# Optimization experiments

Measured on AMD Instinct MI355X. Metric: run time of the kernel, lower is better.

## Reference

```python
import math
import jax, jax.numpy as jnp
import numpy as np

B, Q, K = 1, 2048, 2048
CQ = CK = CV = 128
H, CH = 8, 32
HD = H * CH  # 256


def setup_inputs() -> dict:
    key = jax.random.key(0)
    ks = jax.random.split(key, 12)
    s = 0.02
    return {
        "q_x": jax.random.normal(ks[0], (B, Q, CQ), jnp.float32),
        "kv_x": jax.random.normal(ks[1], (B, K, CK), jnp.float32),
        "bias": jax.random.normal(ks[2], (B, 1, Q, K), jnp.float32),
        "distance": jax.random.uniform(ks[3], (B, Q, K, H), jnp.float32),
        "Wq": jax.random.normal(ks[4], (CQ, HD), jnp.float32) * s,
        "Wk": jax.random.normal(ks[5], (CK, HD), jnp.float32) * s,
        "Wv": jax.random.normal(ks[6], (CV, HD), jnp.float32) * s,
        "Wg": jax.random.normal(ks[7], (CQ, HD), jnp.float32) * s,
        "bg": jnp.zeros((HD,), jnp.float32),
        "Wo": jax.random.normal(ks[8], (HD, CQ), jnp.float32) * s,
        "bo": jnp.zeros((CQ,), jnp.float32),
    }


def reference(q_x, kv_x, bias, distance, Wq, Wk, Wv, Wg, bg, Wo, bo):
    # Projections -> [B, S, H, CH]
    q = (q_x @ Wq).reshape(B, Q, H, CH) / math.sqrt(CH)
    k = (kv_x @ Wk).reshape(B, K, H, CH)
    v = (kv_x @ Wv).reshape(B, K, H, CH)
    # Scores [B, H, Q, K]
    a = jnp.einsum("bqhc,bkhc->bhqk", q, k)
    a = a + bias
    # mha_permu=True: distance [B,Q,K,H] -> [B,H,Q,K]; rel_dis_pair_bias='add'
    a = a + jnp.transpose(distance, (0, 3, 1, 2))
    a = jax.nn.softmax(a, axis=-1)
    o = jnp.einsum("bhqk,bkhc->bqhc", a, v)  # [B, Q, H, CH]
    # Gating
    g = jax.nn.sigmoid(q_x @ Wg + bg).reshape(B, Q, H, CH)
    o = o * g
    o = o.reshape(B, Q, HD)
    return o @ Wo + bo
```

## Files before the change

### kernel.cpp

```cpp
#include <hip/hip_runtime.h>
#include <hip/hip_bf16.h>

#define Qn 2048
#define Kn 2048
#define Cin 128
#define Hn 8
#define CHn 32
#define HDn 256
#define NSPLIT 8

typedef __attribute__((ext_vector_type(8))) short short8;
typedef __attribute__((ext_vector_type(4))) float f32x4;

static __device__ __forceinline__ unsigned short f2bf(float f) {
    unsigned int u = __float_as_uint(f);
    u += 0x7fffu + ((u >> 16) & 1u);
    return (unsigned short)(u >> 16);
}

static __device__ __forceinline__ void ld16(const void* g, void* l) {
    __builtin_amdgcn_global_load_lds(
        (const __attribute__((address_space(1))) void*)g,
        (__attribute__((address_space(3))) void*)l, 16, 0, 0);
}

__global__ __launch_bounds__(256) void proj_kernel(
    const float* __restrict__ qx, const float* __restrict__ kvx,
    const float* __restrict__ Wq, const float* __restrict__ Wk,
    const float* __restrict__ Wv, const float* __restrict__ Wg,
    const float* __restrict__ bg,
    unsigned short* __restrict__ qb, unsigned short* __restrict__ kb,
    unsigned short* __restrict__ vtb, float* __restrict__ gb)
{
    const int mat = blockIdx.y;
    const int r0 = blockIdx.x * 8;
    const int j = threadIdx.x;
    const float* A = (mat == 0 || mat == 3) ? qx : kvx;
    const float* W = (mat == 0) ? Wq : (mat == 1) ? Wk : (mat == 2) ? Wv : Wg;
    const float* Ar = A + r0 * Cin;
    float acc[8] = {0.f, 0.f, 0.f, 0.f, 0.f, 0.f, 0.f, 0.f};
    for (int c = 0; c < Cin; ++c) {
        const float w = W[c * HDn + j];
        #pragma unroll
        for (int i = 0; i < 8; ++i)
            acc[i] = fmaf(Ar[i * Cin + c], w, acc[i]);
    }
    if (mat == 0) {
        const float s = 0.17677669529663687f;
        #pragma unroll
        for (int i = 0; i < 8; ++i)
            qb[(r0 + i) * HDn + j] = f2bf(acc[i] * s);
    } else if (mat == 1) {
        #pragma unroll
        for (int i = 0; i < 8; ++i)
            kb[(r0 + i) * HDn + j] = f2bf(acc[i]);
    } else if (mat == 2) {
        unsigned short tmp[8];
        #pragma unroll
        for (int i = 0; i < 8; ++i) tmp[i] = f2bf(acc[i]);
        *(short8*)(vtb + (size_t)j * Kn + r0) = *(short8*)tmp;
    } else {
        const float b = bg[j];
        #pragma unroll
        for (int i = 0; i < 8; ++i)
            gb[(r0 + i) * HDn + j] = 1.f / (1.f + __expf(-(acc[i] + b)));
    }
}

__global__ __launch_bounds__(512, 4) void attn_kernel(
    const unsigned short* __restrict__ qb, const unsigned short* __restrict__ kb,
    const unsigned short* __restrict__ vtb,
    const float* __restrict__ bias, const float* __restrict__ dist,
    float* __restrict__ opart, float* __restrict__ lpart)
{
    __shared__ float dlds[2][16][32][8];
    __shared__ float blds[2][16][32];
    __shared__ unsigned short ps[Hn][16][40];

    const int bx = blockIdx.x;
    const int qt = bx >> 3;
    const int sp = bx & 7;
    const int q0 = qt * 16;
    const int k00 = sp * 256;
    const int t = threadIdx.x;
    const int h = t >> 6;
    const int l = t & 63;
    const int g = l >> 4;
    const int n = l & 15;

    const short8 qf = *(const short8*)(qb + (q0 + n) * HDn + h * CHn + g * 8);

    f32x4 o0 = {0.f, 0.f, 0.f, 0.f};
    f32x4 o1 = {0.f, 0.f, 0.f, 0.f};
    float lacc[4] = {0.f, 0.f, 0.f, 0.f};
    unsigned short* psh = &ps[h][0][0];
    const f32x4 z = {0.f, 0.f, 0.f, 0.f};

    const float* dsrcA = dist + (size_t)(q0 + h) * Kn * Hn + l * 4;
    const float* dsrcB = dist + (size_t)(q0 + h + 8) * Kn * Hn + l * 4;
    const float* bsrc  = bias + (size_t)(q0 + h * 8 + (l >> 3)) * Kn + (l & 7) * 4;

    short8 kf[2][2], vf[2][2];

    #define STAGE(buf, kt_) do {                                              \
        const int k0s = k00 + (kt_) * 32;                                     \
        ld16(dsrcA + (size_t)k0s * 8, &dlds[buf][h][0][0]);                   \
        ld16(dsrcB + (size_t)k0s * 8, &dlds[buf][h + 8][0][0]);               \
        if (h < 2) ld16(bsrc + k0s, &blds[buf][h * 8][0]);                    \
    } while (0)

    #define KVLOAD(set, kt_) do {                                             \
        const int k0v = k00 + (kt_) * 32;                                     \
        kf[set][0] = *(const short8*)(kb + (k0v + n) * HDn + h * CHn + g * 8);      \
        kf[set][1] = *(const short8*)(kb + (k0v + 16 + n) * HDn + h * CHn + g * 8); \
        vf[set][0] = *(const short8*)(vtb + (h * CHn + n) * Kn + k0v + g * 8);      \
        vf[set][1] = *(const short8*)(vtb + (h * CHn + 16 + n) * Kn + k0v + g * 8); \
    } while (0)

    KVLOAD(0, 0);
    __builtin_amdgcn_sched_barrier(0);
    STAGE(0, 0);

    #pragma unroll
    for (int kt = 0; kt < 8; ++kt) {
        const int cur = kt & 1;
        asm volatile("s_waitcnt vmcnt(0)\n\ts_barrier" ::: "memory");
        if (kt < 7) {
            KVLOAD(cur ^ 1, kt + 1);
            __builtin_amdgcn_sched_barrier(0);
            STAGE(cur ^ 1, kt + 1);
            __builtin_amdgcn_sched_barrier(0);
        }
        f32x4 sf[2];
        sf[0] = __builtin_amdgcn_mfma_f32_16x16x32_bf16(qf, kf[cur][0], z, 0, 0, 0);
        sf[1] = __builtin_amdgcn_mfma_f32_16x16x32_bf16(qf, kf[cur][1], z, 0, 0, 0);
        #pragma unroll
        for (int kk = 0; kk < 2; ++kk) {
            #pragma unroll
            for (int r = 0; r < 4; ++r) {
                const float p = __expf(sf[kk][r]
                                       + dlds[cur][g * 4 + r][kk * 16 + n][h]
                                       + blds[cur][g * 4 + r][kk * 16 + n]);
                sf[kk][r] = p;
                lacc[r] += p;
                psh[(g * 4 + r) * 40 + kk * 16 + n] = f2bf(p);
            }
        }
        const short8 pf = *(const short8*)(psh + n * 40 + g * 8);
        o0 = __builtin_amdgcn_mfma_f32_16x16x32_bf16(pf, vf[cur][0], o0, 0, 0, 0);
        o1 = __builtin_amdgcn_mfma_f32_16x16x32_bf16(pf, vf[cur][1], o1, 0, 0, 0);
    }
    #undef STAGE
    #undef KVLOAD

    float* op = opart + (size_t)sp * (Qn * HDn);
    #pragma unroll
    for (int r = 0; r < 4; ++r) {
        const int qg = q0 + g * 4 + r;
        op[qg * HDn + h * CHn + n] = o0[r];
        op[qg * HDn + h * CHn + 16 + n] = o1[r];
        float v = lacc[r];
        v += __shfl_xor(v, 1);
        v += __shfl_xor(v, 2);
        v += __shfl_xor(v, 4);
        v += __shfl_xor(v, 8);
        lacc[r] = v;
    }
    if (n == 0) {
        float* lp = lpart + (size_t)sp * (Qn * Hn);
        #pragma unroll
        for (int r = 0; r < 4; ++r)
            lp[(q0 + g * 4 + r) * Hn + h] = lacc[r];
    }
}

__global__ __launch_bounds__(256) void mergeout_kernel(
    const float* __restrict__ opart, const float* __restrict__ lpart,
    const float* __restrict__ gb, const float* __restrict__ Wo,
    const float* __restrict__ bo, float* __restrict__ out)
{
    __shared__ float olds[HDn];
    __shared__ float red[4][128];
    const int q = blockIdx.x;
    const int t = threadIdx.x;
    const int h = t >> 5;
    float s = 0.f;
    #pragma unroll
    for (int sp = 0; sp < NSPLIT; ++sp)
        s += opart[(size_t)sp * (Qn * HDn) + q * HDn + t];
    float lt = 0.f;
    #pragma unroll
    for (int sp = 0; sp < NSPLIT; ++sp)
        lt += lpart[(size_t)sp * (Qn * Hn) + q * Hn + h];
    olds[t] = (s / lt) * gb[q * HDn + t];
    __syncthreads();
    const int p = t & 63;
    const int seg = t >> 6;
    float a0 = 0.f, a1 = 0.f;
    for (int c = seg * 64; c < seg * 64 + 64; ++c) {
        const float ov = olds[c];
        const float2 w = *(const float2*)(Wo + c * Cin + 2 * p);
        a0 = fmaf(ov, w.x, a0);
        a1 = fmaf(ov, w.y, a1);
    }
    red[seg][2 * p] = a0;
    red[seg][2 * p + 1] = a1;
    __syncthreads();
    if (t < 128)
        out[q * Cin + t] = red[0][t] + red[1][t] + red[2][t] + red[3][t] + bo[t];
}

extern "C" void kernel_launch(void* const* d_in, const int* in_sizes, int n_in,
                              void* d_out, int out_size, void* d_ws, size_t ws_size,
                              hipStream_t stream)
{
    const float* qx   = (const float*)d_in[0];
    const float* kvx  = (const float*)d_in[1];
    const float* bias = (const float*)d_in[2];
    const float* dist = (const float*)d_in[3];
    const float* Wq   = (const float*)d_in[4];
    const float* Wk   = (const float*)d_in[5];
    const float* Wv   = (const float*)d_in[6];
    const float* Wg   = (const float*)d_in[7];
    const float* bg   = (const float*)d_in[8];
    const float* Wo   = (const float*)d_in[9];
    const float* bo   = (const float*)d_in[10];
    float* out = (float*)d_out;

    char* w = (char*)d_ws;
    unsigned short* qb  = (unsigned short*)(w);
    unsigned short* kb  = (unsigned short*)(w + (1ull << 20));
    unsigned short* vtb = (unsigned short*)(w + (2ull << 20));
    float* gb    = (float*)(w + (3ull << 20));
    float* opart = (float*)(w + (5ull << 20));
    float* lpart = (float*)(w + (21ull << 20));

    proj_kernel<<<dim3(Qn / 8, 4), 256, 0, stream>>>(qx, kvx, Wq, Wk, Wv, Wg, bg, qb, kb, vtb, gb);
    attn_kernel<<<dim3(128 * NSPLIT), 512, 0, stream>>>(qb, kb, vtb, bias, dist, opart, lpart);
    mergeout_kernel<<<dim3(Qn), 256, 0, stream>>>(opart, lpart, gb, Wo, bo, out);
}
```

Measured before the change: 279.1 us.

## Triple-buffer distance tiles with transposed padded LDS layout and preload bias

Distance tiles are now staged with 4-byte global-to-LDS loads that transpose them into a head-major, padded layout (stride 260). This is meant to remove LDS bank conflicts when each head reads its distance values. The staging is triple-buffered with a two-tile lookahead, and partial vmcnt waits replace full drains so loads overlap compute. The whole 256-key bias slice is loaded once up front. The cost is four times as many load instructions with smaller transfers, plus more LDS use, which could lower occupancy.

Measured after the change: 313.7 us. 1.12x slower.

```diff
diff --git a/kernel.cpp b/kernel.cpp
--- a/kernel.cpp
+++ b/kernel.cpp
@@ -8,6 +8,8 @@
 #define CHn 32
 #define HDn 256
 #define NSPLIT 8
+#define DSTR 260
+#define DBUF (16 * DSTR)
 
 typedef __attribute__((ext_vector_type(8))) short short8;
 typedef __attribute__((ext_vector_type(4))) float f32x4;
@@ -22,6 +24,11 @@
     __builtin_amdgcn_global_load_lds(
         (const __attribute__((address_space(1))) void*)g,
         (__attribute__((address_space(3))) void*)l, 16, 0, 0);
+}
+static __device__ __forceinline__ void ld4(const void* g, void* l) {
+    __builtin_amdgcn_global_load_lds(
+        (const __attribute__((address_space(1))) void*)g,
+        (__attribute__((address_space(3))) void*)l, 4, 0, 0);
 }
 
 __global__ __launch_bounds__(256) void proj_kernel(
@@ -73,8 +80,8 @@
     const float* __restrict__ bias, const float* __restrict__ dist,
     float* __restrict__ opart, float* __restrict__ lpart)
 {
-    __shared__ float dlds[2][16][32][8];
-    __shared__ float blds[2][16][32];
+    __shared__ float dl[3 * DBUF];
+    __shared__ float bl[16 * DSTR];
     __shared__ unsigned short ps[Hn][16][40];
 
     const int bx = blockIdx.x;
@@ -96,56 +103,69 @@
     unsigned short* psh = &ps[h][0][0];
     const f32x4 z = {0.f, 0.f, 0.f, 0.f};
 
-    const float* dsrcA = dist + (size_t)(q0 + h) * Kn * Hn + l * 4;
-    const float* dsrcB = dist + (size_t)(q0 + h + 8) * Kn * Hn + l * 4;
-    const float* bsrc  = bias + (size_t)(q0 + h * 8 + (l >> 3)) * Kn + (l & 7) * 4;
+    const int dloff = (l & 31) * 8 + (l >> 5);
+    const float* dgA = dist + (size_t)(q0 + h) * Kn * Hn;
+    const float* dgB = dist + (size_t)(q0 + h + 8) * Kn * Hn;
 
     short8 kf[2][2], vf[2][2];
 
     #define STAGE(buf, kt_) do {                                              \
-        const int k0s = k00 + (kt_) * 32;                                     \
-        ld16(dsrcA + (size_t)k0s * 8, &dlds[buf][h][0][0]);                   \
-        ld16(dsrcB + (size_t)k0s * 8, &dlds[buf][h + 8][0][0]);               \
-        if (h < 2) ld16(bsrc + k0s, &blds[buf][h * 8][0]);                    \
+        const float* gA_ = dgA + (size_t)(k00 + (kt_) * 32) * Hn + dloff;     \
+        const float* gB_ = dgB + (size_t)(k00 + (kt_) * 32) * Hn + dloff;     \
+        float* lA_ = dl + (buf) * DBUF + h * DSTR;                            \
+        float* lB_ = dl + (buf) * DBUF + (h + 8) * DSTR;                      \
+        _Pragma("unroll") for (int i_ = 0; i_ < 4; ++i_) {                    \
+            ld4(gA_ + 2 * i_, lA_ + i_ * 64);                                 \
+            ld4(gB_ + 2 * i_, lB_ + i_ * 64);                                 \
+        }                                                                     \
     } while (0)
 
     #define KVLOAD(set, kt_) do {                                             \
-        const int k0v = k00 + (kt_) * 32;                                     \
+        const int k0v = k00 + (kt_) * 32;                                      \
         kf[set][0] = *(const short8*)(kb + (k0v + n) * HDn + h * CHn + g * 8);      \
         kf[set][1] = *(const short8*)(kb + (k0v + 16 + n) * HDn + h * CHn + g * 8); \
         vf[set][0] = *(const short8*)(vtb + (h * CHn + n) * Kn + k0v + g * 8);      \
         vf[set][1] = *(const short8*)(vtb + (h * CHn + 16 + n) * Kn + k0v + g * 8); \
     } while (0)
 
+    ld16(bias + (size_t)(q0 + 2 * h) * Kn + k00 + l * 4, bl + (2 * h) * DSTR);
+    ld16(bias + (size_t)(q0 + 2 * h + 1) * Kn + k00 + l * 4, bl + (2 * h + 1) * DSTR);
+    __builtin_amdgcn_sched_barrier(0);
+    STAGE(0, 0);
+    __builtin_amdgcn_sched_barrier(0);
     KVLOAD(0, 0);
     __builtin_amdgcn_sched_barrier(0);
-    STAGE(0, 0);
+    STAGE(1, 1);
+    __builtin_amdgcn_sched_barrier(0);
 
     #pragma unroll
     for (int kt = 0; kt < 8; ++kt) {
+        const int cb = kt % 3;
         const int cur = kt & 1;
-        asm volatile("s_waitcnt vmcnt(0)\n\ts_barrier" ::: "memory");
-        if (kt < 7) {
-            KVLOAD(cur ^ 1, kt + 1);
-            __builtin_amdgcn_sched_barrier(0);
-            STAGE(cur ^ 1, kt + 1);
-            __builtin_amdgcn_sched_barrier(0);
-        }
+        if (kt < 7) asm volatile("s_waitcnt vmcnt(8)\n\ts_barrier" ::: "memory");
+        else        asm volatile("s_waitcnt vmcnt(4)\n\ts_barrier" ::: "memory");
+        if (kt < 7) { KVLOAD(cur ^ 1, kt + 1); __builtin_amdgcn_sched_barrier(0); }
+        if (kt < 6) { STAGE((kt + 2) % 3, kt + 2); __builtin_amdgcn_sched_barrier(0); }
+
         f32x4 sf[2];
         sf[0] = __builtin_amdgcn_mfma_f32_16x16x32_bf16(qf, kf[cur][0], z, 0, 0, 0);
         sf[1] = __builtin_amdgcn_mfma_f32_16x16x32_bf16(qf, kf[cur][1], z, 0, 0, 0);
+
+        const float* dlc = dl + cb * DBUF;
         #pragma unroll
         for (int kk = 0; kk < 2; ++kk) {
             #pragma unroll
             for (int r = 0; r < 4; ++r) {
+                const int q_l = g * 4 + r;
                 const float p = __expf(sf[kk][r]
-                                       + dlds[cur][g * 4 + r][kk * 16 + n][h]
-                                       + blds[cur][g * 4 + r][kk * 16 + n]);
+                                       + dlc[q_l * DSTR + h * 32 + kk * 16 + n]
+                                       + bl[q_l * DSTR + kt * 32 + kk * 16 + n]);
                 sf[kk][r] = p;
                 lacc[r] += p;
-                psh[(g * 4 + r) * 40 + kk * 16 + n] = f2bf(p);
+                psh[q_l * 40 + kk * 16 + n] = f2bf(p);
             }
         }
+
         const short8 pf = *(const short8*)(psh + n * 40 + g * 8);
         o0 = __builtin_amdgcn_mfma_f32_16x16x32_bf16(pf, vf[cur][0], o0, 0, 0, 0);
         o1 = __builtin_amdgcn_mfma_f32_16x16x32_bf16(pf, vf[cur][1], o1, 0, 0, 0);
```

## Triple-buffer distance staging and preload full bias tile once per block

Applied to the files above, without the earlier changes.

The distance tile is now staged into a three-deep LDS ring with a prefetch distance of two iterations. The wait before each barrier uses a partial vmcnt, so loads for later tiles stay in flight during compute instead of draining every iteration. The bias for the block's whole 256-key span is loaded once up front into a padded LDS array, which removes the per-iteration bias loads. LDS use grows (about 65KB vs 33KB before), which could lower occupancy under the 4-blocks-per-CU launch bound. The hand-tuned vmcnt counts must also match the number of outstanding loads exactly.

After: 281.0 us. Within noise of the previous version (+0.7%).

```diff
diff --git a/kernel.cpp b/kernel.cpp
--- a/kernel.cpp
+++ b/kernel.cpp
@@ -8,6 +8,7 @@
 #define CHn 32
 #define HDn 256
 #define NSPLIT 8
+#define BSTR 260
 
 typedef __attribute__((ext_vector_type(8))) short short8;
 typedef __attribute__((ext_vector_type(4))) float f32x4;
@@ -73,8 +74,8 @@
     const float* __restrict__ bias, const float* __restrict__ dist,
     float* __restrict__ opart, float* __restrict__ lpart)
 {
-    __shared__ float dlds[2][16][32][8];
-    __shared__ float blds[2][16][32];
+    __shared__ float dl[3][16][256];
+    __shared__ float bl[16 * BSTR];
     __shared__ unsigned short ps[Hn][16][40];
 
     const int bx = blockIdx.x;
@@ -98,54 +99,60 @@
 
     const float* dsrcA = dist + (size_t)(q0 + h) * Kn * Hn + l * 4;
     const float* dsrcB = dist + (size_t)(q0 + h + 8) * Kn * Hn + l * 4;
-    const float* bsrc  = bias + (size_t)(q0 + h * 8 + (l >> 3)) * Kn + (l & 7) * 4;
 
     short8 kf[2][2], vf[2][2];
 
     #define STAGE(buf, kt_) do {                                              \
-        const int k0s = k00 + (kt_) * 32;                                     \
-        ld16(dsrcA + (size_t)k0s * 8, &dlds[buf][h][0][0]);                   \
-        ld16(dsrcB + (size_t)k0s * 8, &dlds[buf][h + 8][0][0]);               \
-        if (h < 2) ld16(bsrc + k0s, &blds[buf][h * 8][0]);                    \
+        const size_t k8 = (size_t)(k00 + (kt_) * 32) * 8;                     \
+        ld16(dsrcA + k8, &dl[buf][h][0]);                                     \
+        ld16(dsrcB + k8, &dl[buf][h + 8][0]);                                 \
     } while (0)
 
     #define KVLOAD(set, kt_) do {                                             \
-        const int k0v = k00 + (kt_) * 32;                                     \
+        const int k0v = k00 + (kt_) * 32;                                      \
         kf[set][0] = *(const short8*)(kb + (k0v + n) * HDn + h * CHn + g * 8);      \
         kf[set][1] = *(const short8*)(kb + (k0v + 16 + n) * HDn + h * CHn + g * 8); \
         vf[set][0] = *(const short8*)(vtb + (h * CHn + n) * Kn + k0v + g * 8);      \
         vf[set][1] = *(const short8*)(vtb + (h * CHn + 16 + n) * Kn + k0v + g * 8); \
     } while (0)
 
+    ld16(bias + (size_t)(q0 + 2 * h) * Kn + k00 + l * 4, bl + (2 * h) * BSTR);
+    ld16(bias + (size_t)(q0 + 2 * h + 1) * Kn + k00 + l * 4, bl + (2 * h + 1) * BSTR);
+    __builtin_amdgcn_sched_barrier(0);
+    STAGE(0, 0);
+    __builtin_amdgcn_sched_barrier(0);
     KVLOAD(0, 0);
     __builtin_amdgcn_sched_barrier(0);
-    STAGE(0, 0);
+    STAGE(1, 1);
+    __builtin_amdgcn_sched_barrier(0);
 
     #pragma unroll
     for (int kt = 0; kt < 8; ++kt) {
+        const int cb = kt % 3;
         const int cur = kt & 1;
-        asm volatile("s_waitcnt vmcnt(0)\n\ts_barrier" ::: "memory");
-        if (kt < 7) {
-            KVLOAD(cur ^ 1, kt + 1);
-            __builtin_amdgcn_sched_barrier(0);
-            STAGE(cur ^ 1, kt + 1);
-            __builtin_amdgcn_sched_barrier(0);
-        }
+        if (kt < 7) asm volatile("s_waitcnt vmcnt(6)\n\ts_barrier" ::: "memory");
+        else        asm volatile("s_waitcnt vmcnt(4)\n\ts_barrier" ::: "memory");
+        if (kt < 7) { KVLOAD(cur ^ 1, kt + 1); __builtin_amdgcn_sched_barrier(0); }
+        if (kt < 6) { STAGE((kt + 2) % 3, kt + 2); __builtin_amdgcn_sched_barrier(0); }
+
         f32x4 sf[2];
         sf[0] = __builtin_amdgcn_mfma_f32_16x16x32_bf16(qf, kf[cur][0], z, 0, 0, 0);
         sf[1] = __builtin_amdgcn_mfma_f32_16x16x32_bf16(qf, kf[cur][1], z, 0, 0, 0);
+
         #pragma unroll
         for (int kk = 0; kk < 2; ++kk) {
             #pragma unroll
             for (int r = 0; r < 4; ++r) {
+                const int q_l = g * 4 + r;
                 const float p = __expf(sf[kk][r]
-                                       + dlds[cur][g * 4 + r][kk * 16 + n][h]
-                                       + blds[cur][g * 4 + r][kk * 16 + n]);
+                                       + dl[cb][q_l][(kk * 16 + n) * 8 + h]
+                                       + bl[q_l * BSTR + kt * 32 + kk * 16 + n]);
                 sf[kk][r] = p;
                 lacc[r] += p;
-                psh[(g * 4 + r) * 40 + kk * 16 + n] = f2bf(p);
+                psh[q_l * 40 + kk * 16 + n] = f2bf(p);
             }
         }
+
         const short8 pf = *(const short8*)(psh + n * 40 + g * 8);
         o0 = __builtin_amdgcn_mfma_f32_16x16x32_bf16(pf, vf[cur][0], o0, 0, 0, 0);
         o1 = __builtin_amdgcn_mfma_f32_16x16x32_bf16(pf, vf[cur][1], o1, 0, 0, 0);
```
